# Performance work log

Measured on AMD Instinct MI355X. Metric: run time of the kernel, lower is better.

The kernel has to match this reference:

```python
import jax, jax.numpy as jnp
import numpy as np


def setup_inputs() -> dict:
    key = jax.random.key(0)
    inputs = jax.random.normal(key, (8, 2048, 512), dtype=jnp.float32)
    return {"inputs": inputs}


def reference(inputs) -> jnp.ndarray:
    # score[b,i,j] = <x_i, x_j>  (no 1/sqrt(d) scaling in the original)
    score = jnp.einsum("bsd,btd->bst", inputs, inputs)  # [B,S,S]
    distribution = jax.nn.softmax(score, axis=-1)
    # output = distribution @ inputs
    return jnp.einsum("bst,btd->bsd", distribution, inputs)
```

## Files before the change

kernel.cpp:

```cpp
#include <hip/hip_runtime.h>
#include <hip/hip_bf16.h>

#define BATCH 8
#define SEQ   2048
#define DIM   512
#define QB    32
#define KB    64
#define NT    512
#define NKV   (SEQ / KB)

typedef __attribute__((ext_vector_type(8))) short short8;
typedef __attribute__((ext_vector_type(4))) float f32x4;
typedef __attribute__((ext_vector_type(4))) unsigned short ushort4v;

__device__ __forceinline__ unsigned short f2bf(float f) {
    union { float f; unsigned u; } v; v.f = f;
    return (unsigned short)((v.u + 0x7FFFu + ((v.u >> 16) & 1u)) >> 16);
}

__device__ __forceinline__ int swz(int kv) {
    return (8 * (kv & 7)) ^ (16 * ((kv >> 3) & 3)) ^ (64 * ((kv >> 3) & 1));
}

__global__ void to_bf16_kernel(const float* __restrict__ X,
                               unsigned short* __restrict__ Y, int n8) {
    const int i = blockIdx.x * blockDim.x + threadIdx.x;
    if (i >= n8) return;
    const float4 a = ((const float4*)X)[i * 2];
    const float4 b = ((const float4*)X)[i * 2 + 1];
    short8 h;
    h[0] = f2bf(a.x); h[1] = f2bf(a.y); h[2] = f2bf(a.z); h[3] = f2bf(a.w);
    h[4] = f2bf(b.x); h[5] = f2bf(b.y); h[6] = f2bf(b.z); h[7] = f2bf(b.w);
    ((short8*)Y)[i] = h;
}

__device__ __forceinline__ void stage_tile(const unsigned short* __restrict__ Xb,
                                           unsigned short* klds_buf,
                                           int t, int w, int lane) {
    const unsigned short* kp = Xb + (size_t)(t * KB) * DIM;
    #pragma unroll
    for (int k = 0; k < 8; ++k) {
        const int kv = k * 8 + w;
        const int dsrc = (lane * 8) ^ swz(kv);
        const unsigned short* g = kp + (size_t)kv * DIM + dsrc;
        unsigned short* l = klds_buf + kv * DIM;
        __builtin_amdgcn_global_load_lds(
            (__attribute__((address_space(1))) void*)(g),
            (__attribute__((address_space(3))) void*)(l), 16, 0, 0);
    }
}

__global__ __launch_bounds__(NT, 2)
void attn_fwd(const unsigned short* __restrict__ Xbf, float* __restrict__ O) {
    const int b   = blockIdx.x & 7;
    const int qt  = blockIdx.x >> 3;
    const int tid = threadIdx.x;
    const int lane = tid & 63;
    const int w    = tid >> 6;
    const int col  = lane & 15;
    const int kgrp = lane >> 4;

    __shared__ alignas(16) unsigned short Klds[2][KB * DIM];
    __shared__ alignas(16) float Sbuf[QB][KB + 4];
    __shared__ alignas(16) unsigned short Pfrag[2][2][64][8];
    __shared__ float m_s[QB], l_s[QB], fac_s[QB];

    const unsigned short* Xb = Xbf + (size_t)b * SEQ * DIM;

    const int qs = w >> 2;
    const int kc = w & 3;
    short8 qfrag[16];
    {
        const int qrow = qt * QB + qs * 16 + col;
        const unsigned short* qp = Xb + (size_t)qrow * DIM;
        #pragma unroll
        for (int ks = 0; ks < 16; ++ks)
            qfrag[ks] = *(const short8*)(qp + ks * 32 + kgrp * 8);
    }

    if (tid < QB) { m_s[tid] = -INFINITY; l_s[tid] = 0.f; }

    f32x4 oacc[2][4];
    #pragma unroll
    for (int i = 0; i < 2; ++i)
        #pragma unroll
        for (int j = 0; j < 4; ++j)
            oacc[i][j] = (f32x4){0.f, 0.f, 0.f, 0.f};

    stage_tile(Xb, &Klds[0][0], 0, w, lane);
    asm volatile("s_waitcnt vmcnt(0)" ::: "memory");
    __syncthreads();

    for (int t = 0; t < NKV; ++t) {
        const int cur = t & 1;
        if (t + 1 < NKV) stage_tile(Xb, &Klds[cur ^ 1][0], t + 1, w, lane);

        {
            const int kvrow = kc * 16 + col;
            const unsigned short* kbase = &Klds[cur][kvrow * DIM];
            const int sw = swz(kvrow);
            f32x4 sacc = (f32x4){0.f,0.f,0.f,0.f};
            #pragma unroll
            for (int ks = 0; ks < 16; ++ks) {
                short8 kfr = *(const short8*)(kbase + ((ks * 32 + kgrp * 8) ^ sw));
                sacc = __builtin_amdgcn_mfma_f32_16x16x32_bf16(qfrag[ks], kfr, sacc, 0, 0, 0);
            }
            #pragma unroll
            for (int r = 0; r < 4; ++r)
                Sbuf[qs * 16 + kgrp * 4 + r][kc * 16 + col] = sacc[r];
        }
        __syncthreads();

        {
            const int r = tid >> 4;
            const int c = tid & 15;
            float4 sa = *(const float4*)&Sbuf[r][c * 4];
            float mloc = fmaxf(fmaxf(sa.x, sa.y), fmaxf(sa.z, sa.w));
            mloc = fmaxf(mloc, __shfl_xor(mloc, 1));
            mloc = fmaxf(mloc, __shfl_xor(mloc, 2));
            mloc = fmaxf(mloc, __shfl_xor(mloc, 4));
            mloc = fmaxf(mloc, __shfl_xor(mloc, 8));
            const float mold = m_s[r];
            const float mnew = fmaxf(mold, mloc);
            const float fac  = __expf(mold - mnew);
            float p0 = __expf(sa.x - mnew), p1 = __expf(sa.y - mnew);
            float p2 = __expf(sa.z - mnew), p3 = __expf(sa.w - mnew);
            float lsum = (p0 + p1) + (p2 + p3);
            lsum += __shfl_xor(lsum, 1);
            lsum += __shfl_xor(lsum, 2);
            lsum += __shfl_xor(lsum, 4);
            lsum += __shfl_xor(lsum, 8);
            ushort4v p4;
            p4[0] = f2bf(p0); p4[1] = f2bf(p1); p4[2] = f2bf(p2); p4[3] = f2bf(p3);
            *(ushort4v*)&Pfrag[r >> 4][c >> 3][(r & 15) + 16 * ((c >> 1) & 3)][(c & 1) * 4] = p4;
            if (c == 0) {
                m_s[r] = mnew;
                fac_s[r] = fac;
                l_s[r] = l_s[r] * fac + lsum;
            }
        }
        __syncthreads();

        #pragma unroll
        for (int q2 = 0; q2 < 2; ++q2) {
            #pragma unroll
            for (int r = 0; r < 4; ++r) {
                const float f = fac_s[q2 * 16 + kgrp * 4 + r];
                #pragma unroll
                for (int dt = 0; dt < 4; ++dt) oacc[q2][dt][r] *= f;
            }
        }
        #pragma unroll
        for (int kc2 = 0; kc2 < 2; ++kc2) {
            const int kvb = kc2 * 32 + kgrp * 8;
            short8 afr[2];
            #pragma unroll
            for (int q2 = 0; q2 < 2; ++q2)
                afr[q2] = *(const short8*)&Pfrag[q2][kc2][lane][0];
            #pragma unroll
            for (int dt = 0; dt < 4; ++dt) {
                const int d = w * 64 + dt * 16 + col;
                short8 bfr;
                #pragma unroll
                for (int j = 0; j < 8; ++j) {
                    const int kv = kvb + j;
                    bfr[j] = (short)Klds[cur][kv * DIM + (d ^ swz(kv))];
                }
                #pragma unroll
                for (int q2 = 0; q2 < 2; ++q2)
                    oacc[q2][dt] = __builtin_amdgcn_mfma_f32_16x16x32_bf16(afr[q2], bfr, oacc[q2][dt], 0, 0, 0);
            }
        }

        asm volatile("s_waitcnt vmcnt(0)" ::: "memory");
        __syncthreads();
    }

    #pragma unroll
    for (int q2 = 0; q2 < 2; ++q2) {
        #pragma unroll
        for (int r = 0; r < 4; ++r) {
            const int row = q2 * 16 + kgrp * 4 + r;
            const float inv = 1.f / l_s[row];
            float* op = O + ((size_t)b * SEQ + qt * QB + row) * DIM + w * 64 + col;
            #pragma unroll
            for (int dt = 0; dt < 4; ++dt)
                op[dt * 16] = oacc[q2][dt][r] * inv;
        }
    }
}

extern "C" void kernel_launch(void* const* d_in, const int* in_sizes, int n_in,
                              void* d_out, int out_size, void* d_ws, size_t ws_size,
                              hipStream_t stream) {
    const float* X = (const float*)d_in[0];
    float* Out = (float*)d_out;
    unsigned short* Xbf = (unsigned short*)d_ws;

    const int n8 = BATCH * SEQ * DIM / 8;
    hipLaunchKernelGGL(to_bf16_kernel, dim3(n8 / 256), dim3(256), 0, stream, X, Xbf, n8);

    dim3 grid(BATCH * (SEQ / QB));
    dim3 block(NT);
    hipLaunchKernelGGL(attn_fwd, grid, block, 0, stream, Xbf, Out);
}
```

Baseline: 183.1 us.

## Pre-transpose V into a separate bf16 buffer and load vector fragments for PV

```diff
diff --git a/kernel.cpp b/kernel.cpp
--- a/kernel.cpp
+++ b/kernel.cpp
@@ -22,36 +22,73 @@
     return (8 * (kv & 7)) ^ (16 * ((kv >> 3) & 3)) ^ (64 * ((kv >> 3) & 1));
 }
 
-__global__ void to_bf16_kernel(const float* __restrict__ X,
-                               unsigned short* __restrict__ Y, int n8) {
-    const int i = blockIdx.x * blockDim.x + threadIdx.x;
-    if (i >= n8) return;
-    const float4 a = ((const float4*)X)[i * 2];
-    const float4 b = ((const float4*)X)[i * 2 + 1];
-    short8 h;
-    h[0] = f2bf(a.x); h[1] = f2bf(a.y); h[2] = f2bf(a.z); h[3] = f2bf(a.w);
-    h[4] = f2bf(b.x); h[5] = f2bf(b.y); h[6] = f2bf(b.z); h[7] = f2bf(b.w);
-    ((short8*)Y)[i] = h;
-}
-
-__device__ __forceinline__ void stage_tile(const unsigned short* __restrict__ Xb,
-                                           unsigned short* klds_buf,
-                                           int t, int w, int lane) {
+__global__ __launch_bounds__(256)
+void prep_kernel(const float* __restrict__ X,
+                 unsigned short* __restrict__ Xbf,
+                 unsigned short* __restrict__ Xt) {
+    __shared__ unsigned short T[64][72];
+    const int b  = blockIdx.z;
+    const int s0 = blockIdx.x * 64;
+    const int d0 = blockIdx.y * 64;
+    const int tid = threadIdx.x;
+    const float* Xb = X + ((size_t)b * SEQ + s0) * DIM + d0;
+    unsigned short* Yb = Xbf + ((size_t)b * SEQ + s0) * DIM + d0;
+    #pragma unroll
+    for (int r = 0; r < 4; ++r) {
+        const int s = (tid >> 4) + r * 16;
+        const int d = (tid & 15) * 4;
+        float4 v = *(const float4*)(Xb + (size_t)s * DIM + d);
+        ushort4v h;
+        h[0] = f2bf(v.x); h[1] = f2bf(v.y); h[2] = f2bf(v.z); h[3] = f2bf(v.w);
+        *(ushort4v*)(Yb + (size_t)s * DIM + d) = h;
+        *(ushort4v*)&T[s][d] = h;
+    }
+    __syncthreads();
+    {
+        const int d = tid >> 2;
+        const int sc = (tid & 3) * 16;
+        unsigned short buf[16];
+        #pragma unroll
+        for (int j = 0; j < 16; ++j) buf[j] = T[sc + j][d];
+        unsigned short* o = Xt + ((size_t)b * DIM + d0 + d) * SEQ + s0 + sc;
+        *(short8*)(o)     = *(short8*)&buf[0];
+        *(short8*)(o + 8) = *(short8*)&buf[8];
+    }
+}
+
+__device__ __forceinline__ void stage_K(const unsigned short* __restrict__ Xb,
+                                        unsigned short* klds, int t, int w, int lane) {
     const unsigned short* kp = Xb + (size_t)(t * KB) * DIM;
     #pragma unroll
     for (int k = 0; k < 8; ++k) {
         const int kv = k * 8 + w;
         const int dsrc = (lane * 8) ^ swz(kv);
         const unsigned short* g = kp + (size_t)kv * DIM + dsrc;
-        unsigned short* l = klds_buf + kv * DIM;
+        unsigned short* l = klds + kv * DIM;
         __builtin_amdgcn_global_load_lds(
             (__attribute__((address_space(1))) void*)(g),
             (__attribute__((address_space(3))) void*)(l), 16, 0, 0);
     }
 }
 
+__device__ __forceinline__ void stage_V(const unsigned short* __restrict__ Xtb,
+                                        unsigned short* vtlds, int t, int w, int lane) {
+    #pragma unroll
+    for (int k = 0; k < 8; ++k) {
+        const int r = w * 64 + k * 8 + (lane >> 3);
+        const int kvsrc = ((lane & 7) * 8) ^ (8 * (r & 7));
+        const unsigned short* g = Xtb + (size_t)r * SEQ + t * KB + kvsrc;
+        unsigned short* l = vtlds + (w * 64 + k * 8) * KB;
+        __builtin_amdgcn_global_load_lds(
+            (__attribute__((address_space(1))) void*)(g),
+            (__attribute__((address_space(3))) void*)(l), 16, 0, 0);
+    }
+}
+
 __global__ __launch_bounds__(NT, 2)
-void attn_fwd(const unsigned short* __restrict__ Xbf, float* __restrict__ O) {
+void attn_fwd(const unsigned short* __restrict__ Xbf,
+              const unsigned short* __restrict__ Xt,
+              float* __restrict__ O) {
     const int b   = blockIdx.x & 7;
     const int qt  = blockIdx.x >> 3;
     const int tid = threadIdx.x;
@@ -60,12 +97,14 @@
     const int col  = lane & 15;
     const int kgrp = lane >> 4;
 
-    __shared__ alignas(16) unsigned short Klds[2][KB * DIM];
+    __shared__ alignas(16) unsigned short Klds[KB * DIM];
+    __shared__ alignas(16) unsigned short Vtlds[DIM * KB];
     __shared__ alignas(16) float Sbuf[QB][KB + 4];
     __shared__ alignas(16) unsigned short Pfrag[2][2][64][8];
     __shared__ float m_s[QB], l_s[QB], fac_s[QB];
 
-    const unsigned short* Xb = Xbf + (size_t)b * SEQ * DIM;
+    const unsigned short* Xb  = Xbf + (size_t)b * SEQ * DIM;
+    const unsigned short* Xtb = Xt  + (size_t)b * DIM * SEQ;
 
     const int qs = w >> 2;
     const int kc = w & 3;
@@ -87,17 +126,15 @@
         for (int j = 0; j < 4; ++j)
             oacc[i][j] = (f32x4){0.f, 0.f, 0.f, 0.f};
 
-    stage_tile(Xb, &Klds[0][0], 0, w, lane);
-    asm volatile("s_waitcnt vmcnt(0)" ::: "memory");
-    __syncthreads();
-
     for (int t = 0; t < NKV; ++t) {
-        const int cur = t & 1;
-        if (t + 1 < NKV) stage_tile(Xb, &Klds[cur ^ 1][0], t + 1, w, lane);
+        stage_K(Xb,  Klds,  t, w, lane);
+        stage_V(Xtb, Vtlds, t, w, lane);
+        asm volatile("s_waitcnt vmcnt(0)" ::: "memory");
+        __syncthreads();
 
         {
             const int kvrow = kc * 16 + col;
-            const unsigned short* kbase = &Klds[cur][kvrow * DIM];
+            const unsigned short* kbase = &Klds[kvrow * DIM];
             const int sw = swz(kvrow);
             f32x4 sacc = (f32x4){0.f,0.f,0.f,0.f};
             #pragma unroll
@@ -160,19 +197,12 @@
             #pragma unroll
             for (int dt = 0; dt < 4; ++dt) {
                 const int d = w * 64 + dt * 16 + col;
-                short8 bfr;
-                #pragma unroll
-                for (int j = 0; j < 8; ++j) {
-                    const int kv = kvb + j;
-                    bfr[j] = (short)Klds[cur][kv * DIM + (d ^ swz(kv))];
-                }
+                const short8 bfr = *(const short8*)&Vtlds[d * KB + (kvb ^ (8 * (d & 7)))];
                 #pragma unroll
                 for (int q2 = 0; q2 < 2; ++q2)
                     oacc[q2][dt] = __builtin_amdgcn_mfma_f32_16x16x32_bf16(afr[q2], bfr, oacc[q2][dt], 0, 0, 0);
             }
         }
-
-        asm volatile("s_waitcnt vmcnt(0)" ::: "memory");
         __syncthreads();
     }
 
@@ -196,11 +226,12 @@
     const float* X = (const float*)d_in[0];
     float* Out = (float*)d_out;
     unsigned short* Xbf = (unsigned short*)d_ws;
-
-    const int n8 = BATCH * SEQ * DIM / 8;
-    hipLaunchKernelGGL(to_bf16_kernel, dim3(n8 / 256), dim3(256), 0, stream, X, Xbf, n8);
+    unsigned short* Xt  = Xbf + (size_t)BATCH * SEQ * DIM;
+
+    dim3 pgrid(SEQ / 64, DIM / 64, BATCH);
+    hipLaunchKernelGGL(prep_kernel, pgrid, dim3(256), 0, stream, X, Xbf, Xt);
 
     dim3 grid(BATCH * (SEQ / QB));
     dim3 block(NT);
-    hipLaunchKernelGGL(attn_fwd, grid, block, 0, stream, Xbf, Out);
-}
+    hipLaunchKernelGGL(attn_fwd, grid, block, 0, stream, Xbf, Xt, Out);
+}
```

After: 200.6 us. 9.6% more time.
